# Optimization experiments

Measured on AMD Instinct MI355X. Metric: run time of the kernel, lower is better.

The kernel has to match this reference:

```python
import jax, jax.numpy as jnp
import numpy as np

H_IMG = 256; W_IMG = 256; C = 256
WIN = (16, 16); STRIPE = (32, 32); DF = 4; NH = 4
ASZ = (STRIPE[0] // DF, STRIPE[1] // DF)
TS = ((STRIPE[0] + ASZ[0]) // 2, (STRIPE[1] + ASZ[1]) // 2)  # stripe bias table half-size (20,20)


def _win_part(x, ws):
    # (B,H,W,c) -> (B*nW, ws0*ws1, c)
    B, H, W, c = x.shape
    x = x.reshape(B, H // ws[0], ws[0], W // ws[1], ws[1], c)
    return x.transpose(0, 1, 3, 2, 4, 5).reshape(-1, ws[0] * ws[1], c)


def _win_rev(w, ws, H, W):
    c = w.shape[-1]
    B = w.shape[0] // ((H // ws[0]) * (W // ws[1]))
    x = w.reshape(B, H // ws[0], W // ws[1], ws[0], ws[1], c)
    return x.transpose(0, 1, 3, 2, 4, 5).reshape(B, H, W, c)


def _l2n(x):
    # F.normalize(dim=-1)
    return x / jnp.maximum(jnp.linalg.norm(x, axis=-1, keepdims=True), 1e-12)


def _affine(attn, logit_scale, w1, b1, w2, table, index):
    # attn: (B_, nH, N1, N2); AffineTransform with mask=None
    N1, N2 = attn.shape[-2], attn.shape[-1]
    attn = attn * jnp.exp(jnp.minimum(logit_scale, np.log(100.0)))  # clamp max=log(1/0.01)
    bt = jax.nn.relu(table.reshape(-1, 2) @ w1 + b1) @ w2  # (T, nH)
    bias = bt[index.reshape(-1)].reshape(N1, N2, -1).transpose(2, 0, 1)  # (nH,N1,N2)
    return attn + (16.0 * jax.nn.sigmoid(bias))[None]


def _coords(start, size):
    h = np.arange(start[0], start[0] + size[0])
    w = np.arange(start[1], start[1] + size[1])
    return np.stack(np.meshgrid(h, w, indexing='ij')).reshape(2, -1)


def _idx(c1, c2, md):
    d = (c1[:, :, None] - c2[:, None, :]).transpose(1, 2, 0).astype(np.int64)
    return (d[..., 0] + md[0] - 1) * (2 * md[1] - 1) + (d[..., 1] + md[1] - 1)


def _table(ts):
    h = np.arange(-(ts[0] - 1), ts[0], dtype=np.float32) / (ts[0] - 1)
    w = np.arange(-(ts[1] - 1), ts[1], dtype=np.float32) / (ts[1] - 1)
    t = np.stack(np.meshgrid(h, w, indexing='ij'), axis=-1)[None] * 8.0
    return (np.sign(t) * np.log2(np.abs(t) + 1.0) / np.log2(8.0)).astype(np.float32)


def setup_inputs():
    ks = iter(jax.random.split(jax.random.key(0), 32))
    def nrm(shape, s=0.02):
        return jax.random.normal(next(ks), shape, dtype=jnp.float32) * s
    inp = {}
    inp['x'] = jax.random.normal(next(ks), (1, H_IMG * W_IMG, C), dtype=jnp.float32)
    inp['qkv_w'] = nrm((C, 3 * C)); inp['qkv_b'] = nrm((3 * C,))
    inp['anchor_w'] = nrm((C, C // 2)); inp['anchor_b'] = nrm((C // 2,))
    for tag in ['w', 's1', 's2']:
        inp['ls_' + tag] = jnp.full((NH, 1, 1), np.log(10.0), dtype=jnp.float32)
        inp['cpb_w1_' + tag] = nrm((2, 512), 0.1)
        inp['cpb_b1_' + tag] = nrm((512,), 0.1)
        inp['cpb_w2_' + tag] = nrm((512, NH), 0.1)
    inp['proj_w'] = nrm((C, C)); inp['proj_b'] = nrm((C,))
    inp['table_w'] = jnp.asarray(_table(WIN))
    inp['table_s'] = jnp.asarray(_table(TS))
    cw = _coords((0, 0), WIN)
    inp['index_w'] = jnp.asarray(_idx(cw, cw, WIN), dtype=jnp.int32)
    cs = _coords((0, 0), STRIPE)
    st = ((STRIPE[0] - ASZ[0]) // 2, (STRIPE[1] - ASZ[1]) // 2)
    ca = _coords(st, ASZ)
    inp['index_a2w'] = jnp.asarray(_idx(ca, cs, TS), dtype=jnp.int32)
    inp['index_w2a'] = jnp.asarray(_idx(cs, ca, TS), dtype=jnp.int32)
    return inp


def reference(x, qkv_w, qkv_b, anchor_w, anchor_b,
              ls_w, cpb_w1_w, cpb_b1_w, cpb_w2_w,
              ls_s1, cpb_w1_s1, cpb_b1_s1, cpb_w2_s1,
              ls_s2, cpb_w1_s2, cpb_b1_s2, cpb_w2_s2,
              proj_w, proj_b, table_w, table_s,
              index_w, index_a2w, index_w2a):
    B, L, c = x.shape
    qkv = x @ qkv_w + qkv_b               # (B, L, 3C)
    half = 3 * c // 2
    hd = half // 3 // NH                  # head_dim per branch
    # ---- window attention on first half of qkv channels ----
    qw = _win_part(qkv[..., :half].reshape(B, H_IMG, W_IMG, half), WIN)  # (B_, N, 3*C/2)
    B_, N, _ = qw.shape
    q, k, v = qw.reshape(B_, N, 3, NH, hd).transpose(2, 0, 3, 1, 4)
    attn = jnp.einsum('bhnd,bhmd->bhnm', _l2n(q), _l2n(k))
    attn = jax.nn.softmax(_affine(attn, ls_w, cpb_w1_w, cpb_b1_w, cpb_w2_w, table_w, index_w), axis=-1)
    xw = jnp.einsum('bhnm,bhmd->bhnd', attn, v).transpose(0, 2, 1, 3).reshape(B_, N, NH * hd)
    xw = _win_rev(xw, WIN, H_IMG, W_IMG).reshape(B, L, c // 2)
    # ---- anchor projection: AvgPool2d(DF) + Linear(C -> C/2) ----
    xi = x.reshape(B, H_IMG, W_IMG, c)
    pooled = xi.reshape(B, H_IMG // DF, DF, W_IMG // DF, DF, c).mean(axis=(2, 4))
    anchor = pooled @ anchor_w + anchor_b  # (B, H/DF, W/DF, C/2)
    # ---- anchor stripe attention on second half ----
    qs = _win_part(qkv[..., half:].reshape(B, H_IMG, W_IMG, half), STRIPE)  # (Bs, N1, 3*C/2)
    Bs, N1, _ = qs.shape
    anc = _win_part(anchor, ASZ)           # (Bs, N2, C/2)
    N2 = anc.shape[1]
    q, k, v = qs.reshape(Bs, N1, 3, NH, hd).transpose(2, 0, 3, 1, 4)
    anc = anc.reshape(Bs, N2, NH, hd).transpose(0, 2, 1, 3)
    a1 = jnp.einsum('bhnd,bhmd->bhnm', _l2n(anc), _l2n(k))   # (Bs,NH,N2,N1)
    a1 = jax.nn.softmax(_affine(a1, ls_s1, cpb_w1_s1, cpb_b1_s1, cpb_w2_s1, table_s, index_a2w), axis=-1)
    xm = jnp.einsum('bhnm,bhmd->bhnd', a1, v)                # (Bs,NH,N2,hd)
    a2 = jnp.einsum('bhnd,bhmd->bhnm', _l2n(q), _l2n(anc))   # (Bs,NH,N1,N2)
    a2 = jax.nn.softmax(_affine(a2, ls_s2, cpb_w1_s2, cpb_b1_s2, cpb_w2_s2, table_s, index_w2a), axis=-1)
    xs = jnp.einsum('bhnm,bhmd->bhnd', a2, xm).transpose(0, 2, 1, 3).reshape(Bs, N1, NH * hd)
    xs = _win_rev(xs, STRIPE, H_IMG, W_IMG).reshape(B, L, c // 2)
    # ---- merge + output projection ----
    return jnp.concatenate([xw, xs], axis=-1) @ proj_w + proj_b
```

## Files before the change

### kernel.cpp

```cpp
#include <hip/hip_runtime.h>
#include <cstdint>
#include <cstddef>

typedef unsigned short u16;
typedef __attribute__((ext_vector_type(8))) short short8;
typedef __attribute__((ext_vector_type(4))) float floatx4;
typedef __attribute__((ext_vector_type(2))) float floatx2;
typedef __attribute__((ext_vector_type(4))) unsigned int uintx4;
typedef __attribute__((ext_vector_type(2))) unsigned int uintx2;
typedef __attribute__((ext_vector_type(2))) __bf16 bf16x2;

#define LOG2E 1.44269504f

__device__ __forceinline__ float bf2f(u16 u){
  union { unsigned int i; float f; } v; v.i = ((unsigned int)u) << 16; return v.f;
}
__device__ __forceinline__ u16 f2bf(float f){
  union { __bf16 b; u16 u; } v; v.b = (__bf16)f; return v.u;
}
__device__ __forceinline__ unsigned int pk2(float a, float b){
  union { bf16x2 h; unsigned int u; } v;
  v.h = __builtin_convertvector((floatx2){a, b}, bf16x2);
  return v.u;
}
__device__ __forceinline__ void gload16(const void* g, void* l){
  __builtin_amdgcn_global_load_lds((const __attribute__((address_space(1))) unsigned int*)g,
                                   (__attribute__((address_space(3))) unsigned int*)l, 16, 0, 0);
}
__device__ __forceinline__ uintx4 ld8f_bf(const float* g){
  floatx4 u0 = *(const floatx4*)g;
  floatx4 u1 = *(const floatx4*)(g + 4);
  uintx4 w;
  w.x = pk2(u0.x, u0.y); w.y = pk2(u0.z, u0.w);
  w.z = pk2(u1.x, u1.y); w.w = pk2(u1.z, u1.w);
  return w;
}
__device__ __forceinline__ float redq(float v){
  v += __shfl_xor(v, 16); v += __shfl_xor(v, 32);
  return v;
}

__global__ void transpose_w(const float* __restrict__ qkv_w, const float* __restrict__ anchor_w,
                            const float* __restrict__ proj_w,
                            u16* __restrict__ qkvt, u16* __restrict__ anct, u16* __restrict__ projt){
  int id = blockIdx.x*256 + threadIdx.x;
  if (id < 196608){ int k = id / 768, n = id % 768; qkvt[n*256 + k] = f2bf(qkv_w[id]); }
  else if (id < 229376){ int r = id - 196608; int k = r / 128, n = r % 128; anct[n*256 + k] = f2bf(anchor_w[r]); }
  else { int r = id - 229376; int k = r >> 8, n = r & 255; projt[n*256 + k] = f2bf(proj_w[r]); }
}

__global__ void cpb_mlp(const float* __restrict__ tw, const float* __restrict__ ts,
                        const float* __restrict__ w1w, const float* __restrict__ b1w, const float* __restrict__ w2w,
                        const float* __restrict__ w1s1, const float* __restrict__ b1s1, const float* __restrict__ w2s1,
                        const float* __restrict__ w1s2, const float* __restrict__ b1s2, const float* __restrict__ w2s2,
                        float* __restrict__ btw, float* __restrict__ bts1, float* __restrict__ bts2){
  int tag = blockIdx.y;
  const float *tab, *w1, *b1, *w2; float* bt; int T;
  if (tag == 0){ tab = tw; w1 = w1w;  b1 = b1w;  w2 = w2w;  bt = btw;  T = 961; }
  else if (tag == 1){ tab = ts; w1 = w1s1; b1 = b1s1; w2 = w2s1; bt = bts1; T = 1521; }
  else { tab = ts; w1 = w1s2; b1 = b1s2; w2 = w2s2; bt = bts2; T = 1521; }
  __shared__ float sw1[2][512];
  __shared__ float sb1[512];
  __shared__ float sw2[512][4];
  for (int j = threadIdx.x; j < 512; j += 256){
    sw1[0][j] = w1[j]; sw1[1][j] = w1[512 + j]; sb1[j] = b1[j];
    for (int h = 0; h < 4; ++h) sw2[j][h] = w2[j*4 + h];
  }
  __syncthreads();
  int idx = blockIdx.x*256 + threadIdx.x;
  int r = idx >> 2, hh = idx & 3;
  if (r < T){
    float t0 = tab[2*r], t1 = tab[2*r + 1];
    float acc = 0.f;
    for (int j = 0; j < 512; ++j){
      float hj = fmaxf(fmaf(t0, sw1[0][j], fmaf(t1, sw1[1][j], sb1[j])), 0.f);
      acc = fmaf(hj, sw2[j][hh], acc);
    }
    bt[r*4 + hh] = acc;
  }
}

__global__ void bias_gather(const float* __restrict__ btw, const float* __restrict__ bts1,
                            const float* __restrict__ bts2,
                            const int* __restrict__ idxw, const int* __restrict__ idxa2w,
                            const int* __restrict__ idxw2a,
                            const float* __restrict__ lsw, const float* __restrict__ ls1,
                            const float* __restrict__ ls2,
                            float* __restrict__ bw, float* __restrict__ bs1, float* __restrict__ bs2){
  int id = blockIdx.x*256 + threadIdx.x;
  int which = id >> 18;
  int rem = id & 262143;
  int h = rem >> 16, e = rem & 65535;
  const float* bt; const int* ix; float* dst; const float* ls;
  if (which == 0){ bt = btw;  ix = idxw;   dst = bw;  ls = lsw; }
  else if (which == 1){ bt = bts1; ix = idxa2w; dst = bs1; ls = ls1; }
  else { bt = bts2; ix = idxw2a; dst = bs2; ls = ls2; }
  float v = bt[ix[e]*4 + h];
  float scale = exp2f(fminf(ls[h], 4.6051702f) * LOG2E);
  float off = fminf(scale + 16.f, 80.f);
  float sig = 16.f / (1.f + exp2f(-v * LOG2E));
  float out = (sig - off) * LOG2E;
  int idx;
  if (which == 0){
    int q = e >> 8, k = e & 255;
    idx = ((((h*8 + (k>>5))*2 + ((k>>4)&1))*4 + ((k>>2)&3)) << 10) + (q << 2) + (k & 3);
  } else if (which == 1){
    int a = e >> 10, k = e & 1023;
    idx = (((h*64 + (k>>4))*4 + ((k>>2)&3)) << 8) + (a << 2) + (k & 3);
  } else {
    int q = e >> 6, k = e & 63;
    idx = (((h*4 + (k>>4))*4 + ((k>>2)&3)) << 12) + (q << 2) + (k & 3);
  }
  dst[idx] = out;
}

__global__ void avgpool(const float* __restrict__ x, float* __restrict__ pooled){
  int a = blockIdx.x, c = threadIdx.x;
  int ay = a >> 6, ax = a & 63;
  float acc = 0.f;
#pragma unroll
  for (int dy = 0; dy < 4; ++dy)
#pragma unroll
    for (int dx = 0; dx < 4; ++dx)
      acc += x[(size_t)((ay*4 + dy)*256 + ax*4 + dx)*256 + c];
  pooled[(size_t)a*256 + c] = acc * 0.0625f;
}

__launch_bounds__(256, 2)
__global__ void gemm_fused(const float* __restrict__ A, const u16* __restrict__ Bt,
                           const float* __restrict__ bias, u16* __restrict__ C,
                           int NY, int normY){
  __shared__ __align__(16) u16 lsA[32768];
  __shared__ __align__(16) u16 lsB[2][4096];
  const int tid = threadIdx.x, lane = tid & 63, wv = tid >> 6;
  const int lane15 = lane & 15, quad = lane >> 4;
  const int wr = wv >> 1, wc = wv & 1;
  const int m0 = blockIdx.x * 128;
  const int N = NY * 128;
  const int brow = wv*16 + (lane >> 2);
  const int bk = (lane & 3)*8;
  auto stageB = [&](int y, int kw, int buf){
    const u16* bs = Bt + (size_t)(y*128 + brow)*256 + kw*32 + bk;
    char* d = (char*)lsB[buf];
    gload16(bs,            d + wv*1024);
    gload16(bs + 64*256,   d + 4096 + wv*1024);
  };
  stageB(0, 0, 0);
  {
    const int row = tid & 127, kh = tid >> 7;
    const float* ap = A + (size_t)(m0 + row)*256 + kh*128;
#pragma unroll
    for (int i = 0; i < 16; ++i){
      int k8 = kh*16 + i;
      uintx4 w = ld8f_bf(ap + i*8);
      *(uintx4*)(lsA + ((size_t)k8*128 + ((row + k8*2) & 127))*8) = w;
    }
  }
  for (int y = 0; y < NY; ++y){
    floatx4 acc[4][4] = {};
    for (int kw = 0; kw < 8; ++kw){
      const int it = y*8 + kw;
      __syncthreads();
      if (it + 1 < NY*8){
        int nit = it + 1;
        stageB(nit >> 3, nit & 7, nit & 1);
      }
      const char* Bc = (const char*)lsB[it & 1];
      const int k8 = kw*4 + quad;
      short8 a[4], b[4];
#pragma unroll
      for (int i = 0; i < 4; ++i)
        a[i] = *(const short8*)(lsA + ((size_t)k8*128 + ((wr*64 + i*16 + lane15 + k8*2) & 127))*8);
#pragma unroll
      for (int j = 0; j < 4; ++j)
        b[j] = *(const short8*)(Bc + (wc*64 + j*16 + lane15)*64 + quad*16);
#pragma unroll
      for (int i = 0; i < 4; ++i)
#pragma unroll
        for (int j = 0; j < 4; ++j)
          acc[i][j] = __builtin_amdgcn_mfma_f32_16x16x32_bf16(b[j], a[i], acc[i][j], 0, 0, 0);
    }
#pragma unroll
    for (int j = 0; j < 4; ++j){
      floatx4 bz = *(const floatx4*)(bias + y*128 + wc*64 + j*16 + quad*4);
#pragma unroll
      for (int i = 0; i < 4; ++i) acc[i][j] += bz;
    }
    if (y < normY){
#pragma unroll
      for (int i = 0; i < 4; ++i)
#pragma unroll
        for (int jp = 0; jp < 2; ++jp){
          floatx4 s2 = acc[i][jp*2]*acc[i][jp*2] + acc[i][jp*2+1]*acc[i][jp*2+1];
          float ss = (s2.x + s2.y) + (s2.z + s2.w);
          ss = redq(ss);
          float inv = 1.f / fmaxf(sqrtf(ss), 1e-12f);
          acc[i][jp*2]   *= inv;
          acc[i][jp*2+1] *= inv;
        }
    }
#pragma unroll
    for (int i = 0; i < 4; ++i){
      int row = m0 + wr*64 + i*16 + lane15;
#pragma unroll
      for (int j = 0; j < 4; ++j){
        int colb = y*128 + wc*64 + j*16 + quad*4;
        uintx2 w;
        w.x = pk2(acc[i][j][0], acc[i][j][1]);
        w.y = pk2(acc[i][j][2], acc[i][j][3]);
        *(uintx2*)(C + (size_t)row*N + colb) = w;
      }
    }
  }
}

__launch_bounds__(256, 2)
__global__ void gemm_proj(const u16* __restrict__ Ab, const u16* __restrict__ Bt,
                          const float* __restrict__ bias, float* __restrict__ Cout){
  __shared__ __align__(16) u16 lsA[2][4096];
  __shared__ __align__(16) u16 lsB[2][8192];
  const int tid = threadIdx.x, lane = tid & 63, wv = tid >> 6;
  const int lane15 = lane & 15, quad = lane >> 4;
  const int wr = wv >> 1, wc = wv & 1;
  const int m0 = blockIdx.x * 128;
  const int srow = wv*16 + (lane >> 2), sk = (lane & 3)*8;
  const u16* as = Ab + (size_t)(m0 + srow)*256 + sk;
  const u16* bs = Bt + (size_t)srow*256 + sk;
  auto stage = [&](int kw, int buf){
    char* dA = (char*)lsA[buf]; char* dB = (char*)lsB[buf];
    gload16(as + kw*32,             dA + wv*1024);
    gload16(as + 64*256 + kw*32,    dA + 4096  + wv*1024);
    gload16(bs + kw*32,             dB + wv*1024);
    gload16(bs + 64*256 + kw*32,    dB + 4096  + wv*1024);
    gload16(bs + 128*256 + kw*32,   dB + 8192  + wv*1024);
    gload16(bs + 192*256 + kw*32,   dB + 12288 + wv*1024);
  };
  stage(0, 0);
  floatx4 acc[4][8] = {};
  for (int kw = 0; kw < 8; ++kw){
    __syncthreads();
    if (kw < 7) stage(kw + 1, (kw + 1) & 1);
    const char* Ac = (const char*)lsA[kw & 1];
    const char* Bc = (const char*)lsB[kw & 1];
    short8 a[4], b[8];
#pragma unroll
    for (int i = 0; i < 4; ++i)
      a[i] = *(const short8*)(Ac + (wr*64 + i*16 + lane15)*64 + quad*16);
#pragma unroll
    for (int j = 0; j < 8; ++j)
      b[j] = *(const short8*)(Bc + (wc*128 + j*16 + lane15)*64 + quad*16);
#pragma unroll
    for (int i = 0; i < 4; ++i)
#pragma unroll
      for (int j = 0; j < 8; ++j)
        acc[i][j] = __builtin_amdgcn_mfma_f32_16x16x32_bf16(b[j], a[i], acc[i][j], 0, 0, 0);
  }
#pragma unroll
  for (int i = 0; i < 4; ++i){
    int row = m0 + wr*64 + i*16 + lane15;
#pragma unroll
    for (int j = 0; j < 8; ++j){
      int colb = wc*128 + j*16 + quad*4;
      floatx4 bz = *(const floatx4*)(bias + colb);
      floatx4 o = acc[i][j] + bz;
      *(floatx4*)(Cout + (size_t)row*256 + colb) = o;
    }
  }
}

__launch_bounds__(256, 3)
__global__ void win_attn(const u16* __restrict__ qkvh, const float* __restrict__ lsw,
                         const float* __restrict__ biasw, u16* __restrict__ outm){
  __shared__ __align__(16) u16 sm[24576];
  const int tid = threadIdx.x, lane = tid & 63, wv = tid >> 6;
  const int lane15 = lane & 15, quad = lane >> 4;
  const int h = blockIdx.y;
  const int wyl = blockIdx.x >> 4, wx = blockIdx.x & 15;
  u16* Ks = sm;
  u16* Qs = sm + 8192;
  u16* VT = sm + 16384;
  {
    int tok = wv*64 + lane;
    int row = (wyl*16 + (tok >> 4))*256 + wx*16 + (tok & 15);
    const char* src = (const char*)qkvh + (size_t)row*768 + h*64;
#pragma unroll
    for (int kq = 0; kq < 4; ++kq){
      gload16(src + kq*16,        (char*)Qs + wv*1024 + kq*4096);
      gload16(src + 256 + kq*16,  (char*)Ks + wv*1024 + kq*4096);
    }
    int vrow = (wyl*16 + (tid >> 4))*256 + wx*16 + (tid & 15);
    const uintx4* vp = (const uintx4*)((const char*)qkvh + (size_t)vrow*768 + 512 + h*64);
    uintx4 v0 = vp[0], v1 = vp[1], v2 = vp[2], v3 = vp[3];
    unsigned int w[16] = {v0.x,v0.y,v0.z,v0.w, v1.x,v1.y,v1.z,v1.w,
                          v2.x,v2.y,v2.z,v2.w, v3.x,v3.y,v3.z,v3.w};
    u16* vd = VT + (tid >> 3)*256 + (tid & 7);
#pragma unroll
    for (int c = 0; c < 16; ++c){
      vd[(c*2)*8]   = (u16)(w[c] & 0xffffu);
      vd[(c*2+1)*8] = (u16)(w[c] >> 16);
    }
  }
  __syncthreads();
  short8 qf[4];
#pragma unroll
  for (int j = 0; j < 4; ++j)
    qf[j] = *(const short8*)(Qs + quad*2048 + (wv*64 + j*16 + lane15)*8);
  __syncthreads();

  float scale = exp2f(fminf(lsw[h], 4.6051702f) * LOG2E) * LOG2E;
  u16* Pw = Qs + wv*2048;
  const floatx4 zf4 = {0.f, 0.f, 0.f, 0.f};
  floatx4 accO[2][4] = {};
  float lsum[4] = {};

  for (int kc = 0; kc < 8; ++kc){
    floatx4 bia[2][4];
#pragma unroll
    for (int i = 0; i < 2; ++i)
#pragma unroll
      for (int j = 0; j < 4; ++j)
        bia[i][j] = *(const floatx4*)(biasw + ((((h*8 + kc)*2 + i)*4 + quad) << 10)
                                            + ((wv*64 + j*16 + lane15) << 2));
    short8 kf[2];
#pragma unroll
    for (int i = 0; i < 2; ++i)
      kf[i] = *(const short8*)(Ks + quad*2048 + (kc*32 + i*16 + lane15)*8);
#pragma unroll
    for (int i = 0; i < 2; ++i)
#pragma unroll
      for (int j = 0; j < 4; ++j){
        floatx4 sv = __builtin_amdgcn_mfma_f32_16x16x32_bf16(kf[i], qf[j], zf4, 0, 0, 0);
        float p0 = exp2f(fmaf(sv[0], scale, bia[i][j][0]));
        float p1 = exp2f(fmaf(sv[1], scale, bia[i][j][1]));
        float p2 = exp2f(fmaf(sv[2], scale, bia[i][j][2]));
        float p3 = exp2f(fmaf(sv[3], scale, bia[i][j][3]));
        lsum[j] += (p0 + p1) + (p2 + p3);
        uintx2 w; w.x = pk2(p0, p1); w.y = pk2(p2, p3);
        *(uintx2*)(Pw + (i*2 + (quad>>1))*512 + (j*16 + lane15)*8 + (quad&1)*4) = w;
      }
    asm volatile("s_waitcnt lgkmcnt(0)" ::: "memory");
    short8 ptf[4], vtf[2];
#pragma unroll
    for (int j = 0; j < 4; ++j)
      ptf[j] = *(const short8*)(Pw + quad*512 + (j*16 + lane15)*8);
#pragma unroll
    for (int m = 0; m < 2; ++m)
      vtf[m] = *(const short8*)(VT + (kc*4 + quad)*256 + (m*16 + lane15)*8);
#pragma unroll
    for (int m = 0; m < 2; ++m)
#pragma unroll
      for (int j = 0; j < 4; ++j)
        accO[m][j] = __builtin_amdgcn_mfma_f32_16x16x32_bf16(vtf[m], ptf[j], accO[m][j], 0, 0, 0);
  }
  float linv[4];
#pragma unroll
  for (int j = 0; j < 4; ++j) linv[j] = 1.f / redq(lsum[j]);
#pragma unroll
  for (int m = 0; m < 2; ++m)
#pragma unroll
    for (int j = 0; j < 4; ++j){
      int tok = wv*64 + j*16 + lane15;
      int py = wyl*16 + (tok >> 4), px = wx*16 + (tok & 15);
      floatx4 o = accO[m][j] * linv[j];
      uintx2 w; w.x = pk2(o[0], o[1]); w.y = pk2(o[2], o[3]);
      *(uintx2*)(outm + (size_t)(py*256 + px)*256 + h*32 + m*16 + quad*4) = w;
    }
}

__launch_bounds__(256, 3)
__global__ void stripe_xm(const u16* __restrict__ qkvh, const u16* __restrict__ anchor,
                          const float* __restrict__ ls1, const float* __restrict__ bias1,
                          float* __restrict__ gl1, u16* __restrict__ gO){
  __shared__ __align__(16) u16 sm[22528];
  const int tid = threadIdx.x, lane = tid & 63, wv = tid >> 6;
  const int lane15 = lane & 15, quad = lane >> 4;
  const int s = blockIdx.x, h = blockIdx.y, kb = blockIdx.z;
  const int syl = s >> 3, sx = s & 7;
  u16* ANC = sm; u16* VT = sm + 10240; u16* P1T = sm + 14336;
  if (wv == 0){
    int ay = syl*8 + (lane >> 3), ax = sx*8 + (lane & 7);
    const char* asrc = (const char*)anchor + (size_t)(ay*64 + ax)*256 + h*64;
#pragma unroll
    for (int kq = 0; kq < 4; ++kq)
      gload16(asrc + kq*16, (char*)ANC + kq*1024);
  }
  auto stageK = [&](int kc){
    int kkb = kb*512 + kc*128;
    char* KC = (char*)sm + 4096 + (kc & 1)*8192;
#pragma unroll
    for (int hf = 0; hf < 2; ++hf){
      int tok = kkb + hf*64 + lane;
      int row = (syl*32 + (tok >> 5))*256 + sx*32 + (tok & 31);
      gload16((const char*)qkvh + (size_t)row*768 + 256 + h*64 + wv*16,
              KC + wv*2048 + hf*1024);
    }
  };
  stageK(0);
  float scale1 = exp2f(fminf(ls1[h], 4.6051702f) * LOG2E) * LOG2E;
  const floatx4 zf4 = {0.f, 0.f, 0.f, 0.f};
  floatx4 accO1[2] = {};
  float l1 = 0.f;
  for (int kc = 0; kc < 4; ++kc){
    int kkb = kb*512 + kc*128;
    {
      int tok_l = tid >> 1, dh = tid & 1;
      int tok = kkb + tok_l;
      int row = (syl*32 + (tok >> 5))*256 + sx*32 + (tok & 31);
      const uintx4* vp = (const uintx4*)((const char*)qkvh + (size_t)row*768 + 512 + h*64 + dh*32);
      uintx4 v0 = vp[0], v1 = vp[1];
      unsigned int w[8] = {v0.x,v0.y,v0.z,v0.w, v1.x,v1.y,v1.z,v1.w};
      u16* vd = VT + (tok_l >> 3)*256 + dh*128 + (tok_l & 7);
#pragma unroll
      for (int c = 0; c < 8; ++c){
        vd[(c*2)*8]   = (u16)(w[c] & 0xffffu);
        vd[(c*2+1)*8] = (u16)(w[c] >> 16);
      }
    }
    __syncthreads();
    if (kc < 3) stageK(kc + 1);
    const u16* KC = sm + 2048 + (kc & 1)*4096;
    short8 ancf = *(const short8*)(ANC + quad*512 + (wv*16 + lane15)*8);
    floatx4 bia[8];
#pragma unroll
    for (int i = 0; i < 8; ++i)
      bia[i] = *(const floatx4*)(bias1 + (((h*64 + kb*32 + kc*8 + i)*4 + quad) << 8)
                                       + ((wv*16 + lane15) << 2));
#pragma unroll
    for (int i = 0; i < 8; ++i){
      short8 kf = *(const short8*)(KC + quad*1024 + (i*16 + lane15)*8);
      floatx4 sv = __builtin_amdgcn_mfma_f32_16x16x32_bf16(kf, ancf, zf4, 0, 0, 0);
      float p0 = exp2f(fmaf(sv[0], scale1, bia[i][0]));
      float p1 = exp2f(fmaf(sv[1], scale1, bia[i][1]));
      float p2 = exp2f(fmaf(sv[2], scale1, bia[i][2]));
      float p3 = exp2f(fmaf(sv[3], scale1, bia[i][3]));
      l1 += (p0 + p1) + (p2 + p3);
      uintx2 w; w.x = pk2(p0, p1); w.y = pk2(p2, p3);
      *(uintx2*)(P1T + (i*2 + (quad>>1))*512 + (wv*16 + lane15)*8 + (quad&1)*4) = w;
    }
    asm volatile("s_waitcnt lgkmcnt(0)" ::: "memory");
#pragma unroll
    for (int ks = 0; ks < 4; ++ks){
      short8 ptf = *(const short8*)(P1T + (ks*4 + quad)*512 + (wv*16 + lane15)*8);
#pragma unroll
      for (int m = 0; m < 2; ++m){
        short8 vtf = *(const short8*)(VT + (ks*4 + quad)*256 + (m*16 + lane15)*8);
        accO1[m] = __builtin_amdgcn_mfma_f32_16x16x32_bf16(vtf, ptf, accO1[m], 0, 0, 0);
      }
    }
    __syncthreads();
  }
  l1 = redq(l1);
  int ent = (s*4 + h)*2 + kb;
  if (quad == 0) gl1[ent*64 + wv*16 + lane15] = l1;
#pragma unroll
  for (int m = 0; m < 2; ++m){
    uintx2 w; w.x = pk2(accO1[m][0], accO1[m][1]); w.y = pk2(accO1[m][2], accO1[m][3]);
    *(uintx2*)(gO + (size_t)ent*2048 + (wv*16 + lane15)*32 + m*16 + quad*4) = w;
  }
}

__launch_bounds__(256, 3)
__global__ void stripe_xs(const u16* __restrict__ qkvh, const u16* __restrict__ anchor,
                          const float* __restrict__ ls2, const float* __restrict__ bias2,
                          const float* __restrict__ gl1, const u16* __restrict__ gO,
                          u16* __restrict__ outm){
  __shared__ __align__(16) u16 sm[20480];
  const int tid = threadIdx.x, lane = tid & 63, wv = tid >> 6;
  const int lane15 = lane & 15, quad = lane >> 4;
  const int s = blockIdx.x >> 2, qc = blockIdx.x & 3, h = blockIdx.y;
  const int syl = s >> 3, sx = s & 7;
  u16* ANC = sm;
  u16* XMT = sm + 2048;
  u16* QW  = sm + 4096 + wv*2048;
  u16* P2T = sm + 12288 + wv*2048;
  if (wv == 0){
    int ay = syl*8 + (lane >> 3), ax = sx*8 + (lane & 7);
    const char* asrc = (const char*)anchor + (size_t)(ay*64 + ax)*256 + h*64;
#pragma unroll
    for (int kq = 0; kq < 4; ++kq)
      gload16(asrc + kq*16, (char*)ANC + kq*1024);
  }
  {
    int a = tid >> 2, db = (tid & 3)*8;
    int e0 = (s*4 + h)*2;
    float inv = 1.f / (gl1[e0*64 + a] + gl1[(e0 + 1)*64 + a]);
    uintx4 u0 = *(const uintx4*)(gO + (size_t)e0*2048 + a*32 + db);
    uintx4 u1 = *(const uintx4*)(gO + (size_t)(e0 + 1)*2048 + a*32 + db);
    unsigned int w0[4] = {u0.x, u0.y, u0.z, u0.w};
    unsigned int w1[4] = {u1.x, u1.y, u1.z, u1.w};
#pragma unroll
    for (int c = 0; c < 4; ++c){
      float a0 = bf2f((u16)(w0[c] & 0xffffu)) + bf2f((u16)(w1[c] & 0xffffu));
      float a1 = bf2f((u16)(w0[c] >> 16))     + bf2f((u16)(w1[c] >> 16));
      XMT[(a >> 3)*256 + (db + c*2)*8     + (a & 7)] = f2bf(a0 * inv);
      XMT[(a >> 3)*256 + (db + c*2 + 1)*8 + (a & 7)] = f2bf(a1 * inv);
    }
  }
  int tq = qc*256 + wv*64;
  {
    int tok = tq + lane;
    int row = (syl*32 + (tok >> 5))*256 + sx*32 + (tok & 31);
    const char* src = (const char*)qkvh + (size_t)row*768 + h*64;
#pragma unroll
    for (int kq = 0; kq < 4; ++kq)
      gload16(src + kq*16, (char*)QW + kq*1024);
  }
  __syncthreads();
  short8 qf2[4];
#pragma unroll
  for (int j = 0; j < 4; ++j)
    qf2[j] = *(const short8*)(QW + quad*512 + (j*16 + lane15)*8);
  float scale2 = exp2f(fminf(ls2[h], 4.6051702f) * LOG2E) * LOG2E;
  const floatx4 zf4 = {0.f, 0.f, 0.f, 0.f};
  floatx4 accO2[2][4] = {};
  float l2[4] = {};
#pragma unroll
  for (int c = 0; c < 2; ++c){
    floatx4 bia[2][4];
#pragma unroll
    for (int i = 0; i < 2; ++i)
#pragma unroll
      for (int j = 0; j < 4; ++j)
        bia[i][j] = *(const floatx4*)(bias2 + ((((h*4 + c*2 + i)*4 + quad) << 12)
                                             + ((tq + j*16 + lane15) << 2)));
    short8 af[2];
#pragma unroll
    for (int i = 0; i < 2; ++i)
      af[i] = *(const short8*)(ANC + quad*512 + (c*32 + i*16 + lane15)*8);
#pragma unroll
    for (int i = 0; i < 2; ++i)
#pragma unroll
      for (int j = 0; j < 4; ++j){
        floatx4 sv = __builtin_amdgcn_mfma_f32_16x16x32_bf16(af[i], qf2[j], zf4, 0, 0, 0);
        float p0 = exp2f(fmaf(sv[0], scale2, bia[i][j][0]));
        float p1 = exp2f(fmaf(sv[1], scale2, bia[i][j][1]));
        float p2 = exp2f(fmaf(sv[2], scale2, bia[i][j][2]));
        float p3 = exp2f(fmaf(sv[3], scale2, bia[i][j][3]));
        l2[j] += (p0 + p1) + (p2 + p3);
        uintx2 w; w.x = pk2(p0, p1); w.y = pk2(p2, p3);
        *(uintx2*)(P2T + (i*2 + (quad>>1))*512 + (j*16 + lane15)*8 + (quad&1)*4) = w;
      }
    asm volatile("s_waitcnt lgkmcnt(0)" ::: "memory");
    short8 ptf[4], xmf[2];
#pragma unroll
    for (int j = 0; j < 4; ++j)
      ptf[j] = *(const short8*)(P2T + quad*512 + (j*16 + lane15)*8);
#pragma unroll
    for (int m = 0; m < 2; ++m)
      xmf[m] = *(const short8*)(XMT + (c*4 + quad)*256 + (m*16 + lane15)*8);
#pragma unroll
    for (int m = 0; m < 2; ++m)
#pragma unroll
      for (int j = 0; j < 4; ++j)
        accO2[m][j] = __builtin_amdgcn_mfma_f32_16x16x32_bf16(xmf[m], ptf[j], accO2[m][j], 0, 0, 0);
  }
  float linv[4];
#pragma unroll
  for (int j = 0; j < 4; ++j) linv[j] = 1.f / redq(l2[j]);
#pragma unroll
  for (int m = 0; m < 2; ++m)
#pragma unroll
    for (int j = 0; j < 4; ++j){
      int tok = tq + j*16 + lane15;
      int py = syl*32 + (tok >> 5), px = sx*32 + (tok & 31);
      floatx4 o = accO2[m][j] * linv[j];
      uintx2 w; w.x = pk2(o[0], o[1]); w.y = pk2(o[2], o[3]);
      *(uintx2*)(outm + (size_t)(py*256 + px)*256 + 128 + h*32 + m*16 + quad*4) = w;
    }
}

extern "C" void kernel_launch(void* const* d_in, const int* in_sizes, int n_in,
                              void* d_out, int out_size, void* d_ws, size_t ws_size,
                              hipStream_t stream) {
  (void)in_sizes; (void)n_in; (void)out_size; (void)ws_size;
  const float* x        = (const float*)d_in[0];
  const float* qkv_w    = (const float*)d_in[1];
  const float* qkv_b    = (const float*)d_in[2];
  const float* anchor_w = (const float*)d_in[3];
  const float* anchor_b = (const float*)d_in[4];
  const float* ls_w     = (const float*)d_in[5];
  const float* w1_w     = (const float*)d_in[6];
  const float* b1_w     = (const float*)d_in[7];
  const float* w2_w     = (const float*)d_in[8];
  const float* ls_s1    = (const float*)d_in[9];
  const float* w1_s1    = (const float*)d_in[10];
  const float* b1_s1    = (const float*)d_in[11];
  const float* w2_s1    = (const float*)d_in[12];
  const float* ls_s2    = (const float*)d_in[13];
  const float* w1_s2    = (const float*)d_in[14];
  const float* b1_s2    = (const float*)d_in[15];
  const float* w2_s2    = (const float*)d_in[16];
  const float* proj_w   = (const float*)d_in[17];
  const float* proj_b   = (const float*)d_in[18];
  const float* table_w  = (const float*)d_in[19];
  const float* table_s  = (const float*)d_in[20];
  const int* index_w   = (const int*)d_in[21];
  const int* index_a2w = (const int*)d_in[22];
  const int* index_w2a = (const int*)d_in[23];

  char* ws = (char*)d_ws;
  u16*   qkvhW  = (u16*)(ws + 0);
  u16*   qkvhS  = (u16*)(ws + 50331648);
  u16*   mergedb= (u16*)(ws + 100663296);
  float* pooled = (float*)(ws + 134217728);
  u16*   anch   = (u16*)(ws + 138412032);
  u16*   qkvt   = (u16*)(ws + 139460608);
  u16*   anct   = (u16*)(ws + 139853824);
  u16*   projt  = (u16*)(ws + 139919360);
  float* btw    = (float*)(ws + 140050432);
  float* bts1   = (float*)(ws + 140066816);
  float* bts2   = (float*)(ws + 140091392);
  float* biasw  = (float*)(ws + 140115968);
  float* bias1  = (float*)(ws + 141164544);
  float* bias2  = (float*)(ws + 142213120);
  float* gl1    = (float*)(ws + 143261696);
  u16*   gO     = (u16*)(ws + 143392768);

  transpose_w<<<1152, 256, 0, stream>>>(qkv_w, anchor_w, proj_w, qkvt, anct, projt);
  cpb_mlp<<<dim3(24, 3), 256, 0, stream>>>(table_w, table_s,
                                           w1_w, b1_w, w2_w,
                                           w1_s1, b1_s1, w2_s1,
                                           w1_s2, b1_s2, w2_s2,
                                           btw, bts1, bts2);
  bias_gather<<<3072, 256, 0, stream>>>(btw, bts1, bts2, index_w, index_a2w, index_w2a,
                                        ls_w, ls_s1, ls_s2, biasw, bias1, bias2);
  avgpool<<<4096, 256, 0, stream>>>(x, pooled);
  gemm_fused<<<32, 256, 0, stream>>>(pooled, anct, anchor_b, anch, 1, 1);
  gemm_fused<<<512, 256, 0, stream>>>(x, qkvt, qkv_b, qkvhW, 3, 2);
  win_attn<<<dim3(256, 4), 256, 0, stream>>>(qkvhW, ls_w, biasw, mergedb);
  gemm_fused<<<512, 256, 0, stream>>>(x, qkvt + 384*256, qkv_b + 384, qkvhS, 3, 2);
  stripe_xm<<<dim3(64, 4, 2), 256, 0, stream>>>(qkvhS, anch, ls_s1, bias1, gl1, gO);
  stripe_xs<<<dim3(256, 4), 256, 0, stream>>>(qkvhS, anch, ls_s2, bias2, gl1, gO, mergedb);
  gemm_proj<<<512, 256, 0, stream>>>(mergedb, projt, proj_b, (float*)d_out);
}
```

Measured before the change: 351.2 us.

## Pre-convert x to bf16 in avgpool and merge QKV GEMMs into one 2D-grid launch

The avgpool kernel now also writes a bf16 copy of x, and a new gemm_bf kernel streams bf16 A and B tiles through double-buffered LDS with async global-to-LDS loads. The two QKV GEMM launches (window and stripe halves) become one launch with a 2D grid, where each block computes one 128-column slice. Before, each block reconverted a full fp32 128x256 A tile and looped over three output slices. The change aims to cut fp32 read traffic, improve parallelism and load overlap, and drop one launch, at the cost of an extra 32MB bf16 write of x. The V-transpose LDS strides in win_attn and stripe_xm are also padded to avoid bank conflicts.

```diff
diff --git a/kernel.cpp b/kernel.cpp
--- a/kernel.cpp
+++ b/kernel.cpp
@@ -26,14 +26,6 @@
 __device__ __forceinline__ void gload16(const void* g, void* l){
   __builtin_amdgcn_global_load_lds((const __attribute__((address_space(1))) unsigned int*)g,
                                    (__attribute__((address_space(3))) unsigned int*)l, 16, 0, 0);
-}
-__device__ __forceinline__ uintx4 ld8f_bf(const float* g){
-  floatx4 u0 = *(const floatx4*)g;
-  floatx4 u1 = *(const floatx4*)(g + 4);
-  uintx4 w;
-  w.x = pk2(u0.x, u0.y); w.y = pk2(u0.z, u0.w);
-  w.z = pk2(u1.x, u1.y); w.w = pk2(u1.z, u1.w);
-  return w;
 }
 __device__ __forceinline__ float redq(float v){
   v += __shfl_xor(v, 16); v += __shfl_xor(v, 32);
@@ -114,102 +106,95 @@
   dst[idx] = out;
 }
 
-__global__ void avgpool(const float* __restrict__ x, float* __restrict__ pooled){
+__global__ void avgpool(const float* __restrict__ x, u16* __restrict__ xb,
+                        u16* __restrict__ pooledb){
   int a = blockIdx.x, c = threadIdx.x;
   int ay = a >> 6, ax = a & 63;
   float acc = 0.f;
 #pragma unroll
   for (int dy = 0; dy < 4; ++dy)
 #pragma unroll
-    for (int dx = 0; dx < 4; ++dx)
-      acc += x[(size_t)((ay*4 + dy)*256 + ax*4 + dx)*256 + c];
-  pooled[(size_t)a*256 + c] = acc * 0.0625f;
+    for (int dx = 0; dx < 4; ++dx){
+      int row = (ay*4 + dy)*256 + ax*4 + dx;
+      float v = x[(size_t)row*256 + c];
+      xb[(size_t)row*256 + c] = f2bf(v);
+      acc += v;
+    }
+  pooledb[(size_t)a*256 + c] = f2bf(acc * 0.0625f);
 }
 
 __launch_bounds__(256, 2)
-__global__ void gemm_fused(const float* __restrict__ A, const u16* __restrict__ Bt,
-                           const float* __restrict__ bias, u16* __restrict__ C,
-                           int NY, int normY){
-  __shared__ __align__(16) u16 lsA[32768];
+__global__ void gemm_bf(const u16* __restrict__ A, const u16* __restrict__ Bt,
+                        const float* __restrict__ bias, u16* __restrict__ CW,
+                        u16* __restrict__ CS, int Nstr, int nyb, int normSl){
+  __shared__ __align__(16) u16 lsA[2][4096];
   __shared__ __align__(16) u16 lsB[2][4096];
   const int tid = threadIdx.x, lane = tid & 63, wv = tid >> 6;
   const int lane15 = lane & 15, quad = lane >> 4;
   const int wr = wv >> 1, wc = wv & 1;
   const int m0 = blockIdx.x * 128;
-  const int N = NY * 128;
-  const int brow = wv*16 + (lane >> 2);
-  const int bk = (lane & 3)*8;
-  auto stageB = [&](int y, int kw, int buf){
-    const u16* bs = Bt + (size_t)(y*128 + brow)*256 + kw*32 + bk;
-    char* d = (char*)lsB[buf];
-    gload16(bs,            d + wv*1024);
-    gload16(bs + 64*256,   d + 4096 + wv*1024);
+  const int y = blockIdx.y;
+  const int br = y / nyb, sl = y - br*nyb;
+  u16* C = br ? CS : CW;
+  const int srow = wv*16 + (lane >> 2), sk = (lane & 3)*8;
+  const u16* as = A + (size_t)(m0 + srow)*256 + sk;
+  const u16* bs = Bt + (size_t)(y*128 + srow)*256 + sk;
+  auto stage = [&](int kw, int buf){
+    char* dA = (char*)lsA[buf]; char* dB = (char*)lsB[buf];
+    gload16(as + kw*32,            dA + wv*1024);
+    gload16(as + 64*256 + kw*32,   dA + 4096 + wv*1024);
+    gload16(bs + kw*32,            dB + wv*1024);
+    gload16(bs + 64*256 + kw*32,   dB + 4096 + wv*1024);
   };
-  stageB(0, 0, 0);
-  {
-    const int row = tid & 127, kh = tid >> 7;
-    const float* ap = A + (size_t)(m0 + row)*256 + kh*128;
-#pragma unroll
-    for (int i = 0; i < 16; ++i){
-      int k8 = kh*16 + i;
-      uintx4 w = ld8f_bf(ap + i*8);
-      *(uintx4*)(lsA + ((size_t)k8*128 + ((row + k8*2) & 127))*8) = w;
-    }
-  }
-  for (int y = 0; y < NY; ++y){
-    floatx4 acc[4][4] = {};
-    for (int kw = 0; kw < 8; ++kw){
-      const int it = y*8 + kw;
-      __syncthreads();
-      if (it + 1 < NY*8){
-        int nit = it + 1;
-        stageB(nit >> 3, nit & 7, nit & 1);
+  stage(0, 0);
+  floatx4 acc[4][4] = {};
+  for (int kw = 0; kw < 8; ++kw){
+    __syncthreads();
+    if (kw < 7) stage(kw + 1, (kw + 1) & 1);
+    const char* Ac = (const char*)lsA[kw & 1];
+    const char* Bc = (const char*)lsB[kw & 1];
+    short8 a[4], b[4];
+#pragma unroll
+    for (int i = 0; i < 4; ++i)
+      a[i] = *(const short8*)(Ac + (wr*64 + i*16 + lane15)*64 + quad*16);
+#pragma unroll
+    for (int j = 0; j < 4; ++j)
+      b[j] = *(const short8*)(Bc + (wc*64 + j*16 + lane15)*64 + quad*16);
+#pragma unroll
+    for (int i = 0; i < 4; ++i)
+#pragma unroll
+      for (int j = 0; j < 4; ++j)
+        acc[i][j] = __builtin_amdgcn_mfma_f32_16x16x32_bf16(b[j], a[i], acc[i][j], 0, 0, 0);
+  }
+#pragma unroll
+  for (int j = 0; j < 4; ++j){
+    floatx4 bz = *(const floatx4*)(bias + y*128 + wc*64 + j*16 + quad*4);
+#pragma unroll
+    for (int i = 0; i < 4; ++i) acc[i][j] += bz;
+  }
+  if (sl < normSl){
+#pragma unroll
+    for (int i = 0; i < 4; ++i)
+#pragma unroll
+      for (int jp = 0; jp < 2; ++jp){
+        floatx4 s2 = acc[i][jp*2]*acc[i][jp*2] + acc[i][jp*2+1]*acc[i][jp*2+1];
+        float ss = (s2.x + s2.y) + (s2.z + s2.w);
+        ss = redq(ss);
+        float inv = 1.f / fmaxf(sqrtf(ss), 1e-12f);
+        acc[i][jp*2]   *= inv;
+        acc[i][jp*2+1] *= inv;
       }
-      const char* Bc = (const char*)lsB[it & 1];
-      const int k8 = kw*4 + quad;
-      short8 a[4], b[4];
-#pragma unroll
-      for (int i = 0; i < 4; ++i)
-        a[i] = *(const short8*)(lsA + ((size_t)k8*128 + ((wr*64 + i*16 + lane15 + k8*2) & 127))*8);
-#pragma unroll
-      for (int j = 0; j < 4; ++j)
-        b[j] = *(const short8*)(Bc + (wc*64 + j*16 + lane15)*64 + quad*16);
-#pragma unroll
-      for (int i = 0; i < 4; ++i)
-#pragma unroll
-        for (int j = 0; j < 4; ++j)
-          acc[i][j] = __builtin_amdgcn_mfma_f32_16x16x32_bf16(b[j], a[i], acc[i][j], 0, 0, 0);
-    }
+  }
+#pragma unroll
+  for (int i = 0; i < 4; ++i){
+    int row = m0 + wr*64 + i*16 + lane15;
 #pragma unroll
     for (int j = 0; j < 4; ++j){
-      floatx4 bz = *(const floatx4*)(bias + y*128 + wc*64 + j*16 + quad*4);
-#pragma unroll
-      for (int i = 0; i < 4; ++i) acc[i][j] += bz;
-    }
-    if (y < normY){
-#pragma unroll
-      for (int i = 0; i < 4; ++i)
-#pragma unroll
-        for (int jp = 0; jp < 2; ++jp){
-          floatx4 s2 = acc[i][jp*2]*acc[i][jp*2] + acc[i][jp*2+1]*acc[i][jp*2+1];
-          float ss = (s2.x + s2.y) + (s2.z + s2.w);
-          ss = redq(ss);
-          float inv = 1.f / fmaxf(sqrtf(ss), 1e-12f);
-          acc[i][jp*2]   *= inv;
-          acc[i][jp*2+1] *= inv;
-        }
-    }
-#pragma unroll
-    for (int i = 0; i < 4; ++i){
-      int row = m0 + wr*64 + i*16 + lane15;
-#pragma unroll
-      for (int j = 0; j < 4; ++j){
-        int colb = y*128 + wc*64 + j*16 + quad*4;
-        uintx2 w;
-        w.x = pk2(acc[i][j][0], acc[i][j][1]);
-        w.y = pk2(acc[i][j][2], acc[i][j][3]);
-        *(uintx2*)(C + (size_t)row*N + colb) = w;
-      }
+      int colb = sl*128 + wc*64 + j*16 + quad*4;
+      uintx2 w;
+      w.x = pk2(acc[i][j][0], acc[i][j][1]);
+      w.y = pk2(acc[i][j][2], acc[i][j][3]);
+      *(uintx2*)(C + (size_t)row*Nstr + colb) = w;
     }
   }
 }
@@ -271,7 +256,7 @@
 __launch_bounds__(256, 3)
 __global__ void win_attn(const u16* __restrict__ qkvh, const float* __restrict__ lsw,
                          const float* __restrict__ biasw, u16* __restrict__ outm){
-  __shared__ __align__(16) u16 sm[24576];
+  __shared__ __align__(16) u16 sm[24832];
   const int tid = threadIdx.x, lane = tid & 63, wv = tid >> 6;
   const int lane15 = lane & 15, quad = lane >> 4;
   const int h = blockIdx.y;
@@ -293,7 +278,7 @@
     uintx4 v0 = vp[0], v1 = vp[1], v2 = vp[2], v3 = vp[3];
     unsigned int w[16] = {v0.x,v0.y,v0.z,v0.w, v1.x,v1.y,v1.z,v1.w,
                           v2.x,v2.y,v2.z,v2.w, v3.x,v3.y,v3.z,v3.w};
-    u16* vd = VT + (tid >> 3)*256 + (tid & 7);
+    u16* vd = VT + (tid >> 3)*264 + (tid & 7);
 #pragma unroll
     for (int c = 0; c < 16; ++c){
       vd[(c*2)*8]   = (u16)(w[c] & 0xffffu);
@@ -345,7 +330,7 @@
       ptf[j] = *(const short8*)(Pw + quad*512 + (j*16 + lane15)*8);
 #pragma unroll
     for (int m = 0; m < 2; ++m)
-      vtf[m] = *(const short8*)(VT + (kc*4 + quad)*256 + (m*16 + lane15)*8);
+      vtf[m] = *(const short8*)(VT + (kc*4 + quad)*264 + (m*16 + lane15)*8);
 #pragma unroll
     for (int m = 0; m < 2; ++m)
 #pragma unroll
@@ -371,12 +356,12 @@
 __global__ void stripe_xm(const u16* __restrict__ qkvh, const u16* __restrict__ anchor,
                           const float* __restrict__ ls1, const float* __restrict__ bias1,
                           float* __restrict__ gl1, u16* __restrict__ gO){
-  __shared__ __align__(16) u16 sm[22528];
+  __shared__ __align__(16) u16 sm[22784];
   const int tid = threadIdx.x, lane = tid & 63, wv = tid >> 6;
   const int lane15 = lane & 15, quad = lane >> 4;
   const int s = blockIdx.x, h = blockIdx.y, kb = blockIdx.z;
   const int syl = s >> 3, sx = s & 7;
-  u16* ANC = sm; u16* VT = sm + 10240; u16* P1T = sm + 14336;
+  u16* ANC = sm; u16* VT = sm + 10240; u16* P1T = sm + 14592;
   if (wv == 0){
     int ay = syl*8 + (lane >> 3), ax = sx*8 + (lane & 7);
     const char* asrc = (const char*)anchor + (size_t)(ay*64 + ax)*256 + h*64;
@@ -409,7 +394,7 @@
       const uintx4* vp = (const uintx4*)((const char*)qkvh + (size_t)row*768 + 512 + h*64 + dh*32);
       uintx4 v0 = vp[0], v1 = vp[1];
       unsigned int w[8] = {v0.x,v0.y,v0.z,v0.w, v1.x,v1.y,v1.z,v1.w};
-      u16* vd = VT + (tok_l >> 3)*256 + dh*128 + (tok_l & 7);
+      u16* vd = VT + (tok_l >> 3)*272 + dh*136 + (tok_l & 7);
 #pragma unroll
       for (int c = 0; c < 8; ++c){
         vd[(c*2)*8]   = (u16)(w[c] & 0xffffu);
@@ -443,7 +428,7 @@
       short8 ptf = *(const short8*)(P1T + (ks*4 + quad)*512 + (wv*16 + lane15)*8);
 #pragma unroll
       for (int m = 0; m < 2; ++m){
-        short8 vtf = *(const short8*)(VT + (ks*4 + quad)*256 + (m*16 + lane15)*8);
+        short8 vtf = *(const short8*)(VT + (ks*4 + quad)*272 + m*136 + lane15*8);
         accO1[m] = __builtin_amdgcn_mfma_f32_16x16x32_bf16(vtf, ptf, accO1[m], 0, 0, 0);
       }
     }
@@ -602,19 +587,20 @@
   u16*   qkvhW  = (u16*)(ws + 0);
   u16*   qkvhS  = (u16*)(ws + 50331648);
   u16*   mergedb= (u16*)(ws + 100663296);
-  float* pooled = (float*)(ws + 134217728);
-  u16*   anch   = (u16*)(ws + 138412032);
-  u16*   qkvt   = (u16*)(ws + 139460608);
-  u16*   anct   = (u16*)(ws + 139853824);
-  u16*   projt  = (u16*)(ws + 139919360);
-  float* btw    = (float*)(ws + 140050432);
-  float* bts1   = (float*)(ws + 140066816);
-  float* bts2   = (float*)(ws + 140091392);
-  float* biasw  = (float*)(ws + 140115968);
-  float* bias1  = (float*)(ws + 141164544);
-  float* bias2  = (float*)(ws + 142213120);
-  float* gl1    = (float*)(ws + 143261696);
-  u16*   gO     = (u16*)(ws + 143392768);
+  u16*   xb     = (u16*)(ws + 134217728);
+  u16*   pooledb= (u16*)(ws + 167772160);
+  u16*   anch   = (u16*)(ws + 169869312);
+  u16*   qkvt   = (u16*)(ws + 170917888);
+  u16*   anct   = (u16*)(ws + 171311104);
+  u16*   projt  = (u16*)(ws + 171376640);
+  float* btw    = (float*)(ws + 171507712);
+  float* bts1   = (float*)(ws + 171524096);
+  float* bts2   = (float*)(ws + 171548672);
+  float* biasw  = (float*)(ws + 171573248);
+  float* bias1  = (float*)(ws + 172621824);
+  float* bias2  = (float*)(ws + 173670400);
+  float* gl1    = (float*)(ws + 174718976);
+  u16*   gO     = (u16*)(ws + 174850048);
 
   transpose_w<<<1152, 256, 0, stream>>>(qkv_w, anchor_w, proj_w, qkvt, anct, projt);
   cpb_mlp<<<dim3(24, 3), 256, 0, stream>>>(table_w, table_s,
@@ -624,11 +610,10 @@
                                            btw, bts1, bts2);
   bias_gather<<<3072, 256, 0, stream>>>(btw, bts1, bts2, index_w, index_a2w, index_w2a,
                                         ls_w, ls_s1, ls_s2, biasw, bias1, bias2);
-  avgpool<<<4096, 256, 0, stream>>>(x, pooled);
-  gemm_fused<<<32, 256, 0, stream>>>(pooled, anct, anchor_b, anch, 1, 1);
-  gemm_fused<<<512, 256, 0, stream>>>(x, qkvt, qkv_b, qkvhW, 3, 2);
+  avgpool<<<4096, 256, 0, stream>>>(x, xb, pooledb);
+  gemm_bf<<<dim3(32, 1), 256, 0, stream>>>(pooledb, anct, anchor_b, anch, anch, 128, 1, 1);
+  gemm_bf<<<dim3(512, 6), 256, 0, stream>>>(xb, qkvt, qkv_b, qkvhW, qkvhS, 384, 3, 2);
   win_attn<<<dim3(256, 4), 256, 0, stream>>>(qkvhW, ls_w, biasw, mergedb);
-  gemm_fused<<<512, 256, 0, stream>>>(x, qkvt + 384*256, qkv_b + 384, qkvhS, 3, 2);
   stripe_xm<<<dim3(64, 4, 2), 256, 0, stream>>>(qkvhS, anch, ls_s1, bias1, gl1, gO);
   stripe_xs<<<dim3(256, 4), 256, 0, stream>>>(qkvhS, anch, ls_s2, bias2, gl1, gO, mergedb);
   gemm_proj<<<512, 256, 0, stream>>>(mergedb, projt, proj_b, (float*)d_out);
```

Result: no change. 351.0 us (-0.0%).
